# Performance work log

Measured on AMD Instinct MI355X. Metric: run time of the kernel, lower is better.

The kernel has to match this reference:

```python
import jax, jax.numpy as jnp
import numpy as np

N = 65536
E = 1048576
IN_DIM, HID, OUT = 500, 256, 64
ALPHA = 0.1
K = 10


def setup_inputs() -> dict:
    key = jax.random.key(0)
    ks = jax.random.split(key, 12)
    x = jax.random.normal(ks[0], (N, IN_DIM), dtype=jnp.float32)
    edge_row = jax.random.randint(ks[1], (E,), 0, N, dtype=jnp.int32)
    edge_col = jax.random.randint(ks[2], (E,), 0, N, dtype=jnp.int32)
    edge_weight = jax.random.uniform(ks[3], (E,), dtype=jnp.float32)
    # Linear params (Kaiming-uniform-like scale)
    def lin(k, fan_in, fan_out):
        kw, kb = jax.random.split(k)
        bound = 1.0 / np.sqrt(fan_in)
        W = jax.random.uniform(kw, (fan_in, fan_out), minval=-bound, maxval=bound, dtype=jnp.float32)
        b = jax.random.uniform(kb, (fan_out,), minval=-bound, maxval=bound, dtype=jnp.float32)
        return W, b
    W1, b1 = lin(ks[4], IN_DIM, HID)
    W2, b2 = lin(ks[5], HID, HID)
    W3, b3 = lin(ks[6], HID, OUT)
    return {"x": x, "W1": W1, "b1": b1, "W2": W2, "b2": b2,
            "W3": W3, "b3": b3, "edge_weight": edge_weight,
            "edge_row": edge_row, "edge_col": edge_col}


def reference(x, W1, b1, W2, b2, W3, b3, edge_weight, edge_row, edge_col):
    # MLP stack (dropout=0.0, norm_type='none')
    h = jax.nn.relu(x @ W1 + b1)          # [N, HID]
    h = jax.nn.relu(h @ W2 + b2)          # [N, HID]
    h = h @ W3 + b3                        # [N, OUT]
    h0 = h
    w = edge_weight[:, None]               # [E, 1]
    # APPNP: k steps of h = (1-alpha) * (A @ h) + alpha * h0 (SpMM via segment_sum)
    def step(h, _):
        msg = h[edge_col] * w               # [E, OUT] gather + scale
        agg = jax.ops.segment_sum(msg, edge_row, num_segments=N)  # [N, OUT]
        return (1.0 - ALPHA) * agg + ALPHA * h0, None
    h, _ = jax.lax.scan(step, h, None, length=K)
    return h
```

## Files before the change

kernel.cpp:

```cpp
#include <hip/hip_runtime.h>
#include <cstdint>
#include <cstddef>


#define N_NODES   65536
#define N_EDGES   1048576
#define IN_DIM    500
#define IN_PAD    512
#define HID_DIM   256
#define OUT_DIM   64
#define K_STEPS   10

#define NPW   8
#define CAPW  608
#define NCHUNK 16

typedef _Float16 half8 __attribute__((ext_vector_type(8)));
typedef float    f32x4 __attribute__((ext_vector_type(4)));

#define XB_OFF    0ULL
#define HA_OFF    0ULL
#define HB_OFF    33554432ULL
#define H1_OFF    67108864ULL
#define H0_OFF    67108864ULL
#define H2_OFF    100663296ULL
#define CNT2_OFF  100663296ULL
#define RANK_OFF  104857600ULL
#define TOT_OFF   109051904ULL
#define W1T_OFF   134217728ULL
#define W2T_OFF   134479872ULL
#define W3T_OFF   134610944ULL
#define ROWP_OFF  134643712ULL
#define EDG_OFF   135430400ULL

#define HALF_U32  ((size_t)N_NODES * 16)

__device__ __forceinline__ void gload_lds16(const void* g, void* l) {
  __builtin_amdgcn_global_load_lds(
      (const __attribute__((address_space(1))) void*)g,
      (__attribute__((address_space(3))) void*)l, 16, 0, 0);
}

__device__ __forceinline__ unsigned short f2bf_rne(float f) {
  unsigned u = __float_as_uint(f);
  u += 0x7fffu + ((u >> 16) & 1u);
  return (unsigned short)(u >> 16);
}
__device__ __forceinline__ float uaf(int u) {
  return __uint_as_float((unsigned)u);
}
__device__ __forceinline__ float lo16(unsigned v) {
  return __uint_as_float(v << 16);
}
__device__ __forceinline__ float hi16(unsigned v) {
  return __uint_as_float(v & 0xffff0000u);
}

template <int TM, int TN, int WM, int WN, bool RELU, int OMODE>
__global__ __launch_bounds__(256)
void gemm_kernel(const _Float16* __restrict__ A, const _Float16* __restrict__ B,
                 const float* __restrict__ bias, void* __restrict__ Cout,
                 int M, int Nn, int K) {
  static_assert((TM * 8) % 256 == 0 && (TN * 8) % 256 == 0, "tile");
  __shared__ uint4 As[TM * 8];
  __shared__ uint4 Bs[TN * 8];
  const int t    = threadIdx.x;
  const int lane = t & 63;
  const int wave = t >> 6;
  const int wm   = wave / WN;
  const int wn   = wave % WN;
  const int row0 = blockIdx.x * TM;
  const int col0 = blockIdx.y * TN;
  const int l15  = lane & 15;
  const int lq   = lane >> 4;

  f32x4 acc[4][4];
#pragma unroll
  for (int i = 0; i < 4; ++i)
#pragma unroll
    for (int j = 0; j < 4; ++j) acc[i][j] = (f32x4){0.f, 0.f, 0.f, 0.f};

  for (int k0 = 0; k0 < K; k0 += 64) {
#pragma unroll
    for (int i = 0; i < (TM * 8) / 256; ++i) {
      const int c = i * 256 + wave * 64 + lane;
      const int q = c / TM;
      const int r = c % TM;
      gload_lds16(A + (size_t)(row0 + r) * K + (k0 + q * 8),
                  As + i * 256 + wave * 64);
    }
#pragma unroll
    for (int i = 0; i < (TN * 8) / 256; ++i) {
      const int c = i * 256 + wave * 64 + lane;
      const int q = c / TN;
      const int r = c % TN;
      gload_lds16(B + (size_t)(col0 + r) * K + (k0 + q * 8),
                  Bs + i * 256 + wave * 64);
    }
    __syncthreads();
#pragma unroll
    for (int kk = 0; kk < 2; ++kk) {
      const int qa = kk * 4 + lq;
      half8 af[4], bfr[4];
#pragma unroll
      for (int mt = 0; mt < 4; ++mt)
        af[mt] = *((const half8*)(As + (qa * TM + wm * 64 + mt * 16 + l15)));
#pragma unroll
      for (int nt = 0; nt < 4; ++nt)
        bfr[nt] = *((const half8*)(Bs + (qa * TN + wn * 64 + nt * 16 + l15)));
#pragma unroll
      for (int mt = 0; mt < 4; ++mt)
#pragma unroll
        for (int nt = 0; nt < 4; ++nt)
          acc[mt][nt] = __builtin_amdgcn_mfma_f32_16x16x32_f16(
              af[mt], bfr[nt], acc[mt][nt], 0, 0, 0);
    }
    __syncthreads();
  }

#pragma unroll
  for (int mt = 0; mt < 4; ++mt) {
#pragma unroll
    for (int nt = 0; nt < 4; ++nt) {
      const int col = col0 + wn * 64 + nt * 16 + l15;
      const float bv = bias[col];
#pragma unroll
      for (int r = 0; r < 4; ++r) {
        const int row = row0 + wm * 64 + mt * 16 + lq * 4 + r;
        float v = acc[mt][nt][r] + bv;
        if (RELU) v = fmaxf(v, 0.f);
        if (OMODE == 0)
          ((_Float16*)Cout)[(size_t)row * Nn + col] = (_Float16)v;
        else if (OMODE == 1)
          ((unsigned short*)Cout)[(size_t)row * Nn + col] = f2bf_rne(v);
        else if (OMODE == 2)
          ((float*)Cout)[(size_t)row * Nn + col] = v;
        else
          ((unsigned short*)Cout)[(size_t)(col >> 5) * ((size_t)N_NODES * 32) +
                                  (size_t)row * 32 + (col & 31)] = f2bf_rne(v);
      }
    }
  }
}

__global__ void cast_x_kernel(const float* __restrict__ x,
                              _Float16* __restrict__ xb) {
  const int c = blockIdx.x * blockDim.x + threadIdx.x;
  if (c >= N_NODES * (IN_PAD / 8)) return;
  const int row = c >> 6;
  const int c8  = (c & 63) << 3;
  half8 o;
  if (c8 + 8 <= IN_DIM) {
    const float4* p = (const float4*)(x + (size_t)row * IN_DIM + c8);
    const float4 a = p[0], b = p[1];
    o[0] = (_Float16)a.x; o[1] = (_Float16)a.y;
    o[2] = (_Float16)a.z; o[3] = (_Float16)a.w;
    o[4] = (_Float16)b.x; o[5] = (_Float16)b.y;
    o[6] = (_Float16)b.z; o[7] = (_Float16)b.w;
  } else {
#pragma unroll
    for (int j = 0; j < 8; ++j) {
      const float v = (c8 + j < IN_DIM) ? x[(size_t)row * IN_DIM + c8 + j] : 0.f;
      o[j] = (_Float16)v;
    }
  }
  *(half8*)(xb + (size_t)c * 8) = o;
}

__global__ void cast_w_kernel(const float* __restrict__ W,
                              _Float16* __restrict__ Wt, int K, int Kpad,
                              int Nn) {
  const int idx = blockIdx.x * blockDim.x + threadIdx.x;
  if (idx >= Nn * Kpad) return;
  const int n = idx / Kpad;
  const int k = idx % Kpad;
  const float v = (k < K) ? W[(size_t)k * Nn + n] : 0.f;
  Wt[idx] = (_Float16)v;
}

__global__ void hist2_kernel(const int* __restrict__ row,
                             int* __restrict__ cnt2, int* __restrict__ rank,
                             int E) {
  const int e = blockIdx.x * blockDim.x + threadIdx.x;
  if (e < E)
    rank[e] = atomicAdd(&cnt2[(e >> 16) * N_NODES + row[e]], 1);
}

__global__ void scan_tot_kernel(const int* __restrict__ cnt2,
                                int* __restrict__ tot) {
  const int r = blockIdx.x * blockDim.x + threadIdx.x;
  int s = 0;
#pragma unroll
  for (int c = 0; c < NCHUNK; ++c) s += cnt2[c * N_NODES + r];
  tot[r] = s;
}

__global__ void scan_kernel(const int4* __restrict__ counts4,
                            int* __restrict__ rowptr) {
  __shared__ int part[1024];
  const int t = threadIdx.x;
  const int base = t * 16;
  int4 c[16];
  int s = 0;
#pragma unroll
  for (int i = 0; i < 16; ++i) {
    c[i] = counts4[base + i];
    s += c[i].x + c[i].y + c[i].z + c[i].w;
  }
  part[t] = s;
  __syncthreads();
  for (int off = 1; off < 1024; off <<= 1) {
    const int v = (t >= off) ? part[t - off] : 0;
    __syncthreads();
    part[t] += v;
    __syncthreads();
  }
  int run = (t == 0) ? 0 : part[t - 1];
#pragma unroll
  for (int i = 0; i < 16; ++i) {
    int4 r;
    r.x = run; run += c[i].x;
    r.y = run; run += c[i].y;
    r.z = run; run += c[i].z;
    r.w = run; run += c[i].w;
    ((int4*)rowptr)[base + i] = r;
  }
  if (t == 1023) rowptr[N_NODES] = run;
}

__global__ void chunkbase_kernel(int* __restrict__ cnt2,
                                 const int* __restrict__ rowptr) {
  const int r = blockIdx.x * blockDim.x + threadIdx.x;
  int run = rowptr[r];
#pragma unroll
  for (int c = 0; c < NCHUNK; ++c) {
    const int t = cnt2[c * N_NODES + r];
    cnt2[c * N_NODES + r] = run;
    run += t;
  }
}

__global__ void scatter2_kernel(const int* __restrict__ row,
                                const int* __restrict__ col,
                                const float* __restrict__ w,
                                const int* __restrict__ rank,
                                const int* __restrict__ cbase,
                                int2* __restrict__ edges, int E) {
  const int e = blockIdx.x * blockDim.x + threadIdx.x;
  if (e < E) {
    const int pos = cbase[(e >> 16) * N_NODES + row[e]] + rank[e];
    edges[pos] = make_int2(col[e], __float_as_int(w[e]));
  }
}

template <bool OUT_F32>
__global__ __launch_bounds__(256)
void prop_half(const unsigned* __restrict__ hin,
               const unsigned* __restrict__ h0,
               void* __restrict__ hout,
               const int* __restrict__ rowptr,
               const int2* __restrict__ edges) {
  __shared__ int2 eb[4][CAPW];
  const int wave = threadIdx.x >> 6;
  const int lane = threadIdx.x & 63;
  const int grp  = lane >> 4;
  const int lg   = lane & 15;
  const int node0 = (blockIdx.x * 4 + wave) * NPW;

  const int rp  = rowptr[node0 + min(lane, NPW)];
  const int beg = __shfl(rp, 0);
  const int nE  = __shfl(rp, NPW) - beg;
  const int rrel = rp - beg;
  int2* __restrict__ ebw = eb[wave];

  const bool fast = (nE <= CAPW);
  if (fast) {
    for (int i = lane; i < nE; i += 64) ebw[i] = edges[beg + i];
    __builtin_amdgcn_s_waitcnt(0);
  }

  for (int i = 0; i < NPW; ++i) {
    const int nb = __shfl(rrel, i);
    const int ne = __shfl(rrel, i + 1);
    float ax0 = 0.f, ay0 = 0.f, ax1 = 0.f, ay1 = 0.f;
    int j = nb;
    if (fast) {
      for (; j + 16 <= ne; j += 16) {
        const int2 e0 = ebw[j + grp];
        const int2 e1 = ebw[j + 4 + grp];
        const int2 e2 = ebw[j + 8 + grp];
        const int2 e3 = ebw[j + 12 + grp];
        const unsigned v0 = hin[(e0.x << 4) | lg];
        const unsigned v1 = hin[(e1.x << 4) | lg];
        const unsigned v2 = hin[(e2.x << 4) | lg];
        const unsigned v3 = hin[(e3.x << 4) | lg];
        const float w0 = uaf(e0.y), w1 = uaf(e1.y);
        const float w2 = uaf(e2.y), w3 = uaf(e3.y);
        ax0 = fmaf(w0, lo16(v0), ax0); ay0 = fmaf(w0, hi16(v0), ay0);
        ax1 = fmaf(w1, lo16(v1), ax1); ay1 = fmaf(w1, hi16(v1), ay1);
        ax0 = fmaf(w2, lo16(v2), ax0); ay0 = fmaf(w2, hi16(v2), ay0);
        ax1 = fmaf(w3, lo16(v3), ax1); ay1 = fmaf(w3, hi16(v3), ay1);
      }
      for (; j + 4 <= ne; j += 4) {
        const int2 e = ebw[j + grp];
        const unsigned v = hin[(e.x << 4) | lg];
        const float w = uaf(e.y);
        ax0 = fmaf(w, lo16(v), ax0); ay0 = fmaf(w, hi16(v), ay0);
      }
      if (j < ne) {
        const int idx = j + grp;
        const int2 e = ebw[idx < ne ? idx : ne - 1];
        const float w = (idx < ne) ? uaf(e.y) : 0.f;
        const unsigned v = hin[(e.x << 4) | lg];
        ax0 = fmaf(w, lo16(v), ax0); ay0 = fmaf(w, hi16(v), ay0);
      }
    } else {
      for (; j < ne; j += 4) {
        const int idx = j + grp;
        const int2 e = edges[beg + (idx < ne ? idx : ne - 1)];
        const float w = (idx < ne) ? uaf(e.y) : 0.f;
        const unsigned v = hin[(e.x << 4) | lg];
        ax0 = fmaf(w, lo16(v), ax0); ay0 = fmaf(w, hi16(v), ay0);
      }
    }
    float sx = ax0 + ax1;
    float sy = ay0 + ay1;
    sx += __shfl_xor(sx, 16); sx += __shfl_xor(sx, 32);
    sy += __shfl_xor(sy, 16); sy += __shfl_xor(sy, 32);
    const int node = node0 + i;
    const int o = (node << 4) | lg;
    const unsigned h0v = h0[o];
    const float r0 = 0.9f * sx + 0.1f * lo16(h0v);
    const float r1 = 0.9f * sy + 0.1f * hi16(h0v);
    if (grp == 0) {
      if (OUT_F32) {
        ((float2*)((float*)hout + ((size_t)node << 6)))[lg] =
            make_float2(r0, r1);
      } else {
        ((unsigned*)hout)[o] =
            (unsigned)f2bf_rne(r0) | ((unsigned)f2bf_rne(r1) << 16);
      }
    }
  }
}

extern "C" void kernel_launch(void* const* d_in, const int* in_sizes, int n_in,
                              void* d_out, int out_size, void* d_ws,
                              size_t ws_size, hipStream_t stream) {
  const float* x  = (const float*)d_in[0];
  const float* W1 = (const float*)d_in[1];
  const float* b1 = (const float*)d_in[2];
  const float* W2 = (const float*)d_in[3];
  const float* b2 = (const float*)d_in[4];
  const float* W3 = (const float*)d_in[5];
  const float* b3 = (const float*)d_in[6];
  const float* ew = (const float*)d_in[7];
  const int* erow = (const int*)d_in[8];
  const int* ecol = (const int*)d_in[9];

  char* ws = (char*)d_ws;
  _Float16* xb  = (_Float16*)(ws + XB_OFF);
  _Float16* h1  = (_Float16*)(ws + H1_OFF);
  _Float16* h2  = (_Float16*)(ws + H2_OFF);
  _Float16* w1t = (_Float16*)(ws + W1T_OFF);
  _Float16* w2t = (_Float16*)(ws + W2T_OFF);
  _Float16* w3t = (_Float16*)(ws + W3T_OFF);
  unsigned* h0h = (unsigned*)(ws + H0_OFF);
  unsigned* hAh = (unsigned*)(ws + HA_OFF);
  unsigned* hBh = (unsigned*)(ws + HB_OFF);
  int* rowp     = (int*)(ws + ROWP_OFF);
  int* cnt2     = (int*)(ws + CNT2_OFF);
  int* rankb    = (int*)(ws + RANK_OFF);
  int* tot      = (int*)(ws + TOT_OFF);
  int2* edges   = (int2*)(ws + EDG_OFF);
  float* outp   = (float*)d_out;

  hipMemsetAsync(cnt2, 0, NCHUNK * N_NODES * sizeof(int), stream);
  hist2_kernel<<<N_EDGES / 256, 256, 0, stream>>>(erow, cnt2, rankb, N_EDGES);
  scan_tot_kernel<<<N_NODES / 256, 256, 0, stream>>>(cnt2, tot);
  scan_kernel<<<1, 1024, 0, stream>>>((const int4*)tot, rowp);
  chunkbase_kernel<<<N_NODES / 256, 256, 0, stream>>>(cnt2, rowp);
  scatter2_kernel<<<N_EDGES / 256, 256, 0, stream>>>(erow, ecol, ew, rankb,
                                                     cnt2, edges, N_EDGES);

  cast_x_kernel<<<(N_NODES * (IN_PAD / 8)) / 256, 256, 0, stream>>>(x, xb);
  cast_w_kernel<<<(HID_DIM * IN_PAD) / 256, 256, 0, stream>>>(W1, w1t, IN_DIM,
                                                              IN_PAD, HID_DIM);
  cast_w_kernel<<<(HID_DIM * HID_DIM) / 256, 256, 0, stream>>>(
      W2, w2t, HID_DIM, HID_DIM, HID_DIM);
  cast_w_kernel<<<(OUT_DIM * HID_DIM) / 256, 256, 0, stream>>>(
      W3, w3t, HID_DIM, HID_DIM, OUT_DIM);

  gemm_kernel<128, 128, 2, 2, true, 0>
      <<<dim3(N_NODES / 128, HID_DIM / 128), 256, 0, stream>>>(
          xb, w1t, b1, h1, N_NODES, HID_DIM, IN_PAD);
  gemm_kernel<128, 128, 2, 2, true, 0>
      <<<dim3(N_NODES / 128, HID_DIM / 128), 256, 0, stream>>>(
          h1, w2t, b2, h2, N_NODES, HID_DIM, HID_DIM);
  gemm_kernel<256, 64, 4, 1, false, 3>
      <<<dim3(N_NODES / 256, 1), 256, 0, stream>>>(h2, w3t, b3, h0h, N_NODES,
                                                   OUT_DIM, HID_DIM);

  for (int s = 0; s < K_STEPS; ++s) {
    const bool last = (s == K_STEPS - 1);
    const unsigned* hin = (s == 0) ? h0h : ((s - 1) & 1 ? hBh : hAh);
    unsigned* hout = (s & 1) ? hBh : hAh;
    for (int half = 0; half < 2; ++half) {
      const unsigned* hinH = hin + half * HALF_U32;
      const unsigned* h0H  = h0h + half * HALF_U32;
      if (!last)
        prop_half<false><<<N_NODES / (4 * NPW), 256, 0, stream>>>(
            hinH, h0H, hout + half * HALF_U32, rowp, edges);
      else
        prop_half<true><<<N_NODES / (4 * NPW), 256, 0, stream>>>(
            hinH, h0H, outp + half * 32, rowp, edges);
    }
  }
}
```

Baseline: 782.6 us.

## Propagate all 64 features per launch with row-major bf16 node features

Replaces the split propagation, which ran two launches per step over 32-feature column halves, with a single launch per step over full 64-feature rows. The last GEMM now writes row-major bf16, and each half-wave gathers a full 128-byte row per edge, covering 2 edges per lane group instead of 4. This aims to halve the edge-list reads and kernel launches per step and make each gather wider. The trade-off is a larger gathered working set per launch, which may fit the cache worse than the half-width tables did.

```diff
diff --git a/kernel.cpp b/kernel.cpp
--- a/kernel.cpp
+++ b/kernel.cpp
@@ -32,8 +32,6 @@
 #define W3T_OFF   134610944ULL
 #define ROWP_OFF  134643712ULL
 #define EDG_OFF   135430400ULL
-
-#define HALF_U32  ((size_t)N_NODES * 16)
 
 __device__ __forceinline__ void gload_lds16(const void* g, void* l) {
   __builtin_amdgcn_global_load_lds(
@@ -133,11 +131,8 @@
           ((_Float16*)Cout)[(size_t)row * Nn + col] = (_Float16)v;
         else if (OMODE == 1)
           ((unsigned short*)Cout)[(size_t)row * Nn + col] = f2bf_rne(v);
-        else if (OMODE == 2)
+        else
           ((float*)Cout)[(size_t)row * Nn + col] = v;
-        else
-          ((unsigned short*)Cout)[(size_t)(col >> 5) * ((size_t)N_NODES * 32) +
-                                  (size_t)row * 32 + (col & 31)] = f2bf_rne(v);
       }
     }
   }
@@ -255,17 +250,18 @@
 
 template <bool OUT_F32>
 __global__ __launch_bounds__(256)
-void prop_half(const unsigned* __restrict__ hin,
-               const unsigned* __restrict__ h0,
-               void* __restrict__ hout,
-               const int* __restrict__ rowptr,
+void prop_step(const unsigned short* __restrict__ hin,
+               const unsigned short* __restrict__ h0,
+               void* __restrict__ hout, const int* __restrict__ rowptr,
                const int2* __restrict__ edges) {
   __shared__ int2 eb[4][CAPW];
   const int wave = threadIdx.x >> 6;
   const int lane = threadIdx.x & 63;
-  const int grp  = lane >> 4;
-  const int lg   = lane & 15;
+  const int half = lane >> 5;
+  const int lp   = lane & 31;
   const int node0 = (blockIdx.x * 4 + wave) * NPW;
+  const unsigned* __restrict__ hin32 = (const unsigned*)hin;
+  const unsigned* __restrict__ h032  = (const unsigned*)h0;
 
   const int rp  = rowptr[node0 + min(lane, NPW)];
   const int beg = __shfl(rp, 0);
@@ -285,15 +281,15 @@
     float ax0 = 0.f, ay0 = 0.f, ax1 = 0.f, ay1 = 0.f;
     int j = nb;
     if (fast) {
-      for (; j + 16 <= ne; j += 16) {
-        const int2 e0 = ebw[j + grp];
-        const int2 e1 = ebw[j + 4 + grp];
-        const int2 e2 = ebw[j + 8 + grp];
-        const int2 e3 = ebw[j + 12 + grp];
-        const unsigned v0 = hin[(e0.x << 4) | lg];
-        const unsigned v1 = hin[(e1.x << 4) | lg];
-        const unsigned v2 = hin[(e2.x << 4) | lg];
-        const unsigned v3 = hin[(e3.x << 4) | lg];
+      for (; j + 8 <= ne; j += 8) {
+        const int2 e0 = ebw[j + 0 + half];
+        const int2 e1 = ebw[j + 2 + half];
+        const int2 e2 = ebw[j + 4 + half];
+        const int2 e3 = ebw[j + 6 + half];
+        const unsigned v0 = hin32[(e0.x << 5) | lp];
+        const unsigned v1 = hin32[(e1.x << 5) | lp];
+        const unsigned v2 = hin32[(e2.x << 5) | lp];
+        const unsigned v3 = hin32[(e3.x << 5) | lp];
         const float w0 = uaf(e0.y), w1 = uaf(e1.y);
         const float w2 = uaf(e2.y), w3 = uaf(e3.y);
         ax0 = fmaf(w0, lo16(v0), ax0); ay0 = fmaf(w0, hi16(v0), ay0);
@@ -301,43 +297,40 @@
         ax0 = fmaf(w2, lo16(v2), ax0); ay0 = fmaf(w2, hi16(v2), ay0);
         ax1 = fmaf(w3, lo16(v3), ax1); ay1 = fmaf(w3, hi16(v3), ay1);
       }
-      for (; j + 4 <= ne; j += 4) {
-        const int2 e = ebw[j + grp];
-        const unsigned v = hin[(e.x << 4) | lg];
+      for (; j + 2 <= ne; j += 2) {
+        const int2 e = ebw[j + half];
+        const unsigned v = hin32[(e.x << 5) | lp];
         const float w = uaf(e.y);
         ax0 = fmaf(w, lo16(v), ax0); ay0 = fmaf(w, hi16(v), ay0);
       }
       if (j < ne) {
-        const int idx = j + grp;
-        const int2 e = ebw[idx < ne ? idx : ne - 1];
-        const float w = (idx < ne) ? uaf(e.y) : 0.f;
-        const unsigned v = hin[(e.x << 4) | lg];
+        const int2 e = ebw[j];
+        const unsigned v = hin32[(e.x << 5) | lp];
+        const float w = half ? 0.f : uaf(e.y);
         ax0 = fmaf(w, lo16(v), ax0); ay0 = fmaf(w, hi16(v), ay0);
       }
     } else {
-      for (; j < ne; j += 4) {
-        const int idx = j + grp;
+      for (; j < ne; j += 2) {
+        const int idx = j + half;
         const int2 e = edges[beg + (idx < ne ? idx : ne - 1)];
         const float w = (idx < ne) ? uaf(e.y) : 0.f;
-        const unsigned v = hin[(e.x << 4) | lg];
+        const unsigned v = hin32[(e.x << 5) | lp];
         ax0 = fmaf(w, lo16(v), ax0); ay0 = fmaf(w, hi16(v), ay0);
       }
     }
     float sx = ax0 + ax1;
     float sy = ay0 + ay1;
-    sx += __shfl_xor(sx, 16); sx += __shfl_xor(sx, 32);
-    sy += __shfl_xor(sy, 16); sy += __shfl_xor(sy, 32);
-    const int node = node0 + i;
-    const int o = (node << 4) | lg;
-    const unsigned h0v = h0[o];
+    sx += __shfl_xor(sx, 32);
+    sy += __shfl_xor(sy, 32);
+    const int o32 = ((node0 + i) << 5) | lp;
+    const unsigned h0v = h032[o32];
     const float r0 = 0.9f * sx + 0.1f * lo16(h0v);
     const float r1 = 0.9f * sy + 0.1f * hi16(h0v);
-    if (grp == 0) {
+    if (half == 0) {
       if (OUT_F32) {
-        ((float2*)((float*)hout + ((size_t)node << 6)))[lg] =
-            make_float2(r0, r1);
+        ((float2*)hout)[o32] = make_float2(r0, r1);
       } else {
-        ((unsigned*)hout)[o] =
+        ((unsigned*)hout)[o32] =
             (unsigned)f2bf_rne(r0) | ((unsigned)f2bf_rne(r1) << 16);
       }
     }
@@ -365,9 +358,9 @@
   _Float16* w1t = (_Float16*)(ws + W1T_OFF);
   _Float16* w2t = (_Float16*)(ws + W2T_OFF);
   _Float16* w3t = (_Float16*)(ws + W3T_OFF);
-  unsigned* h0h = (unsigned*)(ws + H0_OFF);
-  unsigned* hAh = (unsigned*)(ws + HA_OFF);
-  unsigned* hBh = (unsigned*)(ws + HB_OFF);
+  unsigned short* h0b = (unsigned short*)(ws + H0_OFF);
+  unsigned short* hAb = (unsigned short*)(ws + HA_OFF);
+  unsigned short* hBb = (unsigned short*)(ws + HB_OFF);
   int* rowp     = (int*)(ws + ROWP_OFF);
   int* cnt2     = (int*)(ws + CNT2_OFF);
   int* rankb    = (int*)(ws + RANK_OFF);
@@ -397,23 +390,16 @@
   gemm_kernel<128, 128, 2, 2, true, 0>
       <<<dim3(N_NODES / 128, HID_DIM / 128), 256, 0, stream>>>(
           h1, w2t, b2, h2, N_NODES, HID_DIM, HID_DIM);
-  gemm_kernel<256, 64, 4, 1, false, 3>
-      <<<dim3(N_NODES / 256, 1), 256, 0, stream>>>(h2, w3t, b3, h0h, N_NODES,
+  gemm_kernel<256, 64, 4, 1, false, 1>
+      <<<dim3(N_NODES / 256, 1), 256, 0, stream>>>(h2, w3t, b3, h0b, N_NODES,
                                                    OUT_DIM, HID_DIM);
 
-  for (int s = 0; s < K_STEPS; ++s) {
-    const bool last = (s == K_STEPS - 1);
-    const unsigned* hin = (s == 0) ? h0h : ((s - 1) & 1 ? hBh : hAh);
-    unsigned* hout = (s & 1) ? hBh : hAh;
-    for (int half = 0; half < 2; ++half) {
-      const unsigned* hinH = hin + half * HALF_U32;
-      const unsigned* h0H  = h0h + half * HALF_U32;
-      if (!last)
-        prop_half<false><<<N_NODES / (4 * NPW), 256, 0, stream>>>(
-            hinH, h0H, hout + half * HALF_U32, rowp, edges);
-      else
-        prop_half<true><<<N_NODES / (4 * NPW), 256, 0, stream>>>(
-            hinH, h0H, outp + half * 32, rowp, edges);
-    }
-  }
-}
+  for (int s = 0; s < K_STEPS - 1; ++s) {
+    const unsigned short* hin = (s == 0) ? h0b : ((s - 1) & 1 ? hBb : hAb);
+    unsigned short* hout = (s & 1) ? hBb : hAb;
+    prop_step<false><<<N_NODES / (4 * NPW), 256, 0, stream>>>(hin, h0b, hout,
+                                                              rowp, edges);
+  }
+  prop_step<true><<<N_NODES / (4 * NPW), 256, 0, stream>>>(
+      (K_STEPS - 2) & 1 ? hBb : hAb, h0b, outp, rowp, edges);
+}
```

Result: faster. 641.8 us (-18.0%).
